# Kernel tuning notes

Hardware: AMD Instinct MI355X
Metric: run time of the kernel (lower is better)

Reference implementation:

```python
import jax, jax.numpy as jnp
import numpy as np
import math

HEADS = 4
DIM_HEAD = 32
EPS = 1e-5

def _ln_channels(x):
    # LayerNorm over channel axis (axis=1) of NCHW, no affine (eps=1e-5)
    mu = jnp.mean(x, axis=1, keepdims=True)
    var = jnp.mean((x - mu) ** 2, axis=1, keepdims=True)
    return (x - mu) * jax.lax.rsqrt(var + EPS)

def setup_inputs() -> dict:
    key = jax.random.key(0)
    k1, k2, k3, k4 = jax.random.split(key, 4)
    dim, inner = 256, HEADS * DIM_HEAD
    x = jax.random.normal(k1, (16, dim, 64, 64), dtype=jnp.float32)
    Wqkv = jax.random.normal(k2, (3 * inner, dim), dtype=jnp.float32) * (1.0 / math.sqrt(dim))
    Wout = jax.random.normal(k3, (dim, inner), dtype=jnp.float32) * (1.0 / math.sqrt(inner))
    bout = jax.random.normal(k4, (dim,), dtype=jnp.float32) * 0.01
    return {"x": x, "Wqkv": Wqkv, "Wout": Wout, "bout": bout}

def reference(x, Wqkv, Wout, bout):
    B, C, H, W = x.shape
    N = H * W
    inner = HEADS * DIM_HEAD
    # pre-norm (channel-wise LayerNorm via permute in torch)
    normed = _ln_channels(x)
    # 1x1 conv to qkv: [B, 3*inner, H, W]
    qkv = jnp.einsum('oc,bchw->bohw', Wqkv, normed)
    q, k, v = jnp.split(qkv, 3, axis=1)
    # [B, inner, H, W] -> [B, heads, N, dim_head]
    def to_heads(t):
        return t.reshape(B, HEADS, DIM_HEAD, N).transpose(0, 1, 3, 2)
    q, k, v = to_heads(q), to_heads(k), to_heads(v)
    q = jax.nn.softmax(q, axis=-1)          # over dim_head
    k = jax.nn.softmax(k, axis=-2)          # over N
    q = q / math.sqrt(DIM_HEAD)
    v = v / N
    context = jnp.einsum('bhnd,bhne->bhde', k, v)   # [B,h,d,d]
    out = jnp.einsum('bhde,bhnd->bhne', context, q) # [B,h,N,d]
    out = out.transpose(0, 1, 3, 2).reshape(B, inner, H, W)
    out = jnp.einsum('oc,bchw->bohw', Wout, out) + bout[None, :, None, None]
    out = _ln_channels(out)                  # LinearAttention.out_norm
    return out + x                           # residual
```

## Files before the change

kernel.cpp:

```cpp
#include <hip/hip_runtime.h>
#include <hip/hip_bf16.h>
#include <math.h>

#define BATCH 16
#define CH 256
#define NPOS 4096
#define INNER 128
#define HEADS 4
#define DH 32

typedef __hip_bfloat16 bf16;
typedef short bf8v __attribute__((ext_vector_type(8)));
typedef float f32x4 __attribute__((ext_vector_type(4)));

__device__ __forceinline__ float b2f(bf16 v) { return __bfloat162float(v); }
__device__ __forceinline__ float us2f(unsigned short u) {
    unsigned w = ((unsigned)u) << 16; float f; __builtin_memcpy(&f, &w, 4); return f;
}
__device__ __forceinline__ unsigned short f2us(float f) {
    bf16 h = __float2bfloat16(f); unsigned short u; __builtin_memcpy(&u, &h, 2); return u;
}
__device__ __forceinline__ bf16 f2b(float v) { return __float2bfloat16(v); }

__global__ __launch_bounds__(256)
void fused_qkv_kernel(const float* __restrict__ x, const float* __restrict__ Wqkv,
                      bf16* __restrict__ p, bf16* __restrict__ kvt) {
    __shared__ bf16 A[128 * 264];
    __shared__ bf16 Bb[128 * 32];
    __shared__ float stats[512];

    const int b = blockIdx.y, n0 = blockIdx.x * 128;
    const int tid = threadIdx.x;
    const int wave = tid >> 6, lane = tid & 63;
    const int wm = (wave >> 1) * 64, wn = (wave & 1) * 64;
    const int lrow = lane & 15, kq = lane >> 4;

    {
        const int n = tid & 127, chalf = tid >> 7;
        const float* xp = x + ((size_t)b * CH + chalf * 128) * NPOS + n0 + n;
        float s = 0.f, sq = 0.f;
        for (int i0 = 0; i0 < 128; i0 += 8) {
            bf8v bv;
            #pragma unroll
            for (int j = 0; j < 8; ++j) {
                float v = xp[(size_t)(i0 + j) * NPOS];
                s += v; sq += v * v;
                bv[j] = (short)f2us(v);
            }
            *(bf8v*)&A[n * 264 + chalf * 128 + i0] = bv;
        }
        stats[tid * 2] = s; stats[tid * 2 + 1] = sq;
    }
    __syncthreads();
    if (tid < 128) {
        float s  = stats[tid * 2] + stats[(tid + 128) * 2];
        float sq = stats[tid * 2 + 1] + stats[(tid + 128) * 2 + 1];
        float m = s * (1.f / 256.f);
        float var = sq * (1.f / 256.f) - m * m;
        stats[tid * 2] = m;
        stats[tid * 2 + 1] = rsqrtf(var + 1e-5f);
    }
    __syncthreads();
    {
        unsigned* A32 = (unsigned*)A;
        #pragma unroll 4
        for (int i = 0; i < 64; ++i) {
            int idx = i * 256 + tid;
            int c2 = idx & 127, n = idx >> 7;
            unsigned u = A32[n * 132 + c2];
            float m = stats[n * 2], rs = stats[n * 2 + 1];
            float v0 = (us2f((unsigned short)(u & 0xffffu)) - m) * rs;
            float v1 = (us2f((unsigned short)(u >> 16)) - m) * rs;
            A32[n * 132 + c2] = (unsigned)f2us(v0) | ((unsigned)f2us(v1) << 16);
        }
    }

    for (int ph = 0; ph < 3; ++ph) {
        const int colbase = (ph == 2) ? 0 : (ph + 1) * 128;
        f32x4 acc[4][4];
        #pragma unroll
        for (int i = 0; i < 4; ++i)
            #pragma unroll
            for (int j = 0; j < 4; ++j) acc[i][j] = (f32x4){0.f, 0.f, 0.f, 0.f};

        for (int k0 = 0; k0 < 256; k0 += 32) {
            __syncthreads();
            #pragma unroll
            for (int i = 0; i < 4; ++i) {
                int s = i * 256 + tid;
                int col = s >> 3, q4 = s & 7;
                float4 w = *(const float4*)&Wqkv[(size_t)(colbase + col) * 256 + k0 + q4 * 4];
                ushort4 wb;
                wb.x = f2us(w.x); wb.y = f2us(w.y); wb.z = f2us(w.z); wb.w = f2us(w.w);
                *(ushort4*)&Bb[col * 32 + q4 * 4] = wb;
            }
            __syncthreads();
            bf8v af[4], bfr[4];
            #pragma unroll
            for (int t = 0; t < 4; ++t)
                af[t] = *(const bf8v*)&A[(wm + t * 16 + lrow) * 264 + k0 + kq * 8];
            #pragma unroll
            for (int t = 0; t < 4; ++t)
                bfr[t] = *(const bf8v*)&Bb[(wn + t * 16 + lrow) * 32 + kq * 8];
            #pragma unroll
            for (int mt = 0; mt < 4; ++mt)
                #pragma unroll
                for (int nt = 0; nt < 4; ++nt)
                    acc[mt][nt] = __builtin_amdgcn_mfma_f32_16x16x32_bf16(
                        af[mt], bfr[nt], acc[mt][nt], 0, 0, 0);
        }

        if (ph < 2) {
            unsigned* B32 = (unsigned*)Bb;
            unsigned* kv32 = (unsigned*)kvt;
            for (int pr = 0; pr < 4; ++pr) {
                __syncthreads();
                if ((wave >> 1) == (pr >> 1)) {
                    int mtb = (pr & 1) * 2;
                    #pragma unroll
                    for (int mi = 0; mi < 2; ++mi) {
                        int mt = mtb + mi;
                        #pragma unroll
                        for (int nt = 0; nt < 4; ++nt)
                            #pragma unroll
                            for (int r = 0; r < 4; ++r) {
                                int rl = mi * 16 + kq * 4 + r;
                                Bb[rl * 128 + wn + nt * 16 + lrow] = f2b(acc[mt][nt][r]);
                            }
                    }
                }
                __syncthreads();
                #pragma unroll
                for (int i = 0; i < 8; ++i) {
                    int idx = i * 256 + tid;
                    int c2 = idx & 63, rl = idx >> 6;
                    kv32[(size_t)(b * NPOS + n0 + pr * 32 + rl) * 128 + ph * 64 + c2] =
                        B32[rl * 64 + c2];
                }
            }
        } else {
            __syncthreads();
            bf16* pt = A;
            #pragma unroll
            for (int mt = 0; mt < 4; ++mt)
                #pragma unroll
                for (int nt = 0; nt < 4; ++nt)
                    #pragma unroll
                    for (int r = 0; r < 4; ++r)
                        pt[(wm + mt * 16 + kq * 4 + r) * 132 + wn + nt * 16 + lrow] =
                            f2b(acc[mt][nt][r]);
            __syncthreads();
            {
                int row = tid >> 1, hp = (tid & 1) * 2;
                float s0 = 0.f, s1 = 0.f;
                #pragma unroll 8
                for (int j = 0; j < 32; ++j) s0 += __expf(b2f(pt[row * 132 + hp * 32 + j]));
                #pragma unroll 8
                for (int j = 0; j < 32; ++j) s1 += __expf(b2f(pt[row * 132 + hp * 32 + 32 + j]));
                stats[row * 4 + hp] = 1.f / s0;
                stats[row * 4 + hp + 1] = 1.f / s1;
            }
            __syncthreads();
            unsigned* pt32 = (unsigned*)pt;
            unsigned* pg32 = (unsigned*)p;
            #pragma unroll 4
            for (int i = 0; i < 32; ++i) {
                int idx = i * 256 + tid;
                int c2 = idx & 63, n = idx >> 6;
                unsigned u = pt32[n * 66 + c2];
                float rd = stats[n * 4 + (c2 >> 4)];
                float v0 = __expf(us2f((unsigned short)(u & 0xffffu))) * rd;
                float v1 = __expf(us2f((unsigned short)(u >> 16))) * rd;
                pg32[(size_t)(b * NPOS + n0 + n) * 64 + c2] =
                    (unsigned)f2us(v0) | ((unsigned)f2us(v1) << 16);
            }
        }
    }
}

__global__ __launch_bounds__(256)
void context_kernel(const bf16* __restrict__ kvt, float* __restrict__ ctxu,
                    float* __restrict__ separt) {
    __shared__ float ks[128][36];
    __shared__ float vs[128][36];
    __shared__ float red_se[4][32];
    int sp = blockIdx.x, h = blockIdx.y, b = blockIdx.z;
    int tid = threadIdx.x;
    int wave = tid >> 6, lane = tid & 63;
    int eg = lane & 7, dg = lane >> 3;
    int sd = tid & 31, sq = (tid >> 5) & 3;
    const int koff = h * DH, voff = 128 + h * DH;
    size_t rowbase = ((size_t)b * NPOS + sp * 1024) * 256;

    float acc[4][4] = {};
    float se_loc = 0.f;

    for (int nc = 0; nc < 1024; nc += 128) {
        for (int t = tid; t < 1024; t += 256) {
            int n = t >> 3, dq = t & 7;
            const bf16* row = kvt + rowbase + (size_t)(nc + n) * 256;
            ushort4 ku = *(const ushort4*)(row + koff + dq * 4);
            ushort4 vu = *(const ushort4*)(row + voff + dq * 4);
            f32x4 kf, vf;
            kf[0] = __expf(us2f(ku.x)); kf[1] = __expf(us2f(ku.y));
            kf[2] = __expf(us2f(ku.z)); kf[3] = __expf(us2f(ku.w));
            vf[0] = us2f(vu.x); vf[1] = us2f(vu.y); vf[2] = us2f(vu.z); vf[3] = us2f(vu.w);
            *(f32x4*)&ks[n][dq * 4] = kf;
            *(f32x4*)&vs[n][dq * 4] = vf;
        }
        __syncthreads();
        #pragma unroll 4
        for (int i = 0; i < 32; ++i) {
            int n = wave * 32 + i;
            f32x4 kv = *(const f32x4*)&ks[n][dg * 4];
            f32x4 vv = *(const f32x4*)&vs[n][eg * 4];
            #pragma unroll
            for (int j = 0; j < 4; ++j)
                #pragma unroll
                for (int i2 = 0; i2 < 4; ++i2)
                    acc[j][i2] += kv[j] * vv[i2];
        }
        if (tid < 128) {
            float s = 0.f;
            #pragma unroll 8
            for (int i = 0; i < 32; ++i) s += ks[sq * 32 + i][sd];
            se_loc += s;
        }
        __syncthreads();
    }

    if (tid < 128) red_se[sq][sd] = se_loc;
    float* red = &ks[0][0];
    #pragma unroll
    for (int j = 0; j < 4; ++j)
        #pragma unroll
        for (int i = 0; i < 4; ++i)
            red[(wave * 64 + lane) * 16 + j * 4 + i] = acc[j][i];
    __syncthreads();
    size_t bhsp = ((size_t)(b * HEADS + h) * 4 + sp);
    for (int idx = tid; idx < 1024; idx += 256) {
        int d = idx >> 5, e = idx & 31;
        int l = (d >> 2) * 8 + (e >> 2);
        int slot = (d & 3) * 4 + (e & 3);
        float s = 0.f;
        #pragma unroll
        for (int w = 0; w < 4; ++w) s += red[(w * 64 + l) * 16 + slot];
        ctxu[bhsp * 1024 + idx] = s;
    }
    if (tid < 32) {
        float s = red_se[0][tid] + red_se[1][tid] + red_se[2][tid] + red_se[3][tid];
        separt[bhsp * 32 + tid] = s;
    }
}

__global__ __launch_bounds__(256)
void wmod_kernel(const float* __restrict__ Wout, const float* __restrict__ ctxu,
                 const float* __restrict__ separt, bf16* __restrict__ wmod) {
    __shared__ float cs[4096];
    __shared__ float ses[128];
    int cg = blockIdx.x, b = blockIdx.y;
    int tid = threadIdx.x;
    for (int idx = tid; idx < 4096; idx += 256) {
        int hh = idx >> 10, rest = idx & 1023;
        float s = 0.f;
        #pragma unroll
        for (int sp = 0; sp < 4; ++sp)
            s += ctxu[(((size_t)(b * HEADS + hh) * 4) + sp) * 1024 + rest];
        cs[idx] = s;
    }
    if (tid < 128) {
        int hh = tid >> 5, d = tid & 31;
        float s = 0.f;
        #pragma unroll
        for (int sp = 0; sp < 4; ++sp)
            s += separt[(((size_t)(b * HEADS + hh) * 4) + sp) * 32 + d];
        ses[tid] = s;
    }
    __syncthreads();
    int c = cg * 32 + (tid & 31);
    int g = tid >> 5;
    int h = g >> 1, d0 = (g & 1) * 16;
    const float* wr = Wout + (size_t)c * INNER + h * DH;
    float w[32];
    #pragma unroll
    for (int i = 0; i < 8; ++i) {
        float4 t = *(const float4*)&wr[i * 4];
        w[i * 4] = t.x; w[i * 4 + 1] = t.y; w[i * 4 + 2] = t.z; w[i * 4 + 3] = t.w;
    }
    const float SCALE = 4.3158341e-05f;
    #pragma unroll
    for (int dd = 0; dd < 16; ++dd) {
        int d = d0 + dd;
        const float* cr = &cs[h * 1024 + d * 32];
        float s = 0.f;
        #pragma unroll
        for (int e4 = 0; e4 < 8; ++e4) {
            f32x4 t = *(const f32x4*)&cr[e4 * 4];
            s += w[e4 * 4] * t[0] + w[e4 * 4 + 1] * t[1]
               + w[e4 * 4 + 2] * t[2] + w[e4 * 4 + 3] * t[3];
        }
        float val = s * SCALE / ses[h * 32 + d];
        wmod[((size_t)b * CH + c) * INNER + h * DH + d] = f2b(val);
    }
}

__global__ __launch_bounds__(256)
void fused_out_kernel(const bf16* __restrict__ p, const bf16* __restrict__ wmod,
                      const float* __restrict__ bout, const float* __restrict__ x,
                      float* __restrict__ out) {
    __shared__ char lds[51200];
    bf16* Ap = (bf16*)lds;
    bf16* Bw = (bf16*)(lds + 34816);
    float* ct = (float*)lds;
    float* st = (float*)(lds + 34816);

    const int b = blockIdx.y, n0 = blockIdx.x * 128;
    const int tid = threadIdx.x;
    const int wave = tid >> 6, lane = tid & 63;
    const int wm = (wave >> 1) * 64, wn2 = (wave & 1) * 128;
    const int lrow = lane & 15, kq = lane >> 4;

    {
        const unsigned* pg32 = (const unsigned*)p;
        unsigned* A32 = (unsigned*)Ap;
        #pragma unroll 4
        for (int i = 0; i < 32; ++i) {
            int idx = i * 256 + tid;
            int c2 = idx & 63, n = idx >> 6;
            A32[n * 68 + c2] = pg32[(size_t)(b * NPOS + n0 + n) * 64 + c2];
        }
    }

    f32x4 acc[4][8];
    #pragma unroll
    for (int i = 0; i < 4; ++i)
        #pragma unroll
        for (int j = 0; j < 8; ++j) acc[i][j] = (f32x4){0.f, 0.f, 0.f, 0.f};

    const bf16* wb = wmod + (size_t)b * CH * INNER;
    for (int k0 = 0; k0 < 128; k0 += 32) {
        __syncthreads();
        #pragma unroll
        for (int i = 0; i < 4; ++i) {
            int s = i * 256 + tid;
            int col = s >> 2, q4 = s & 3;
            uint4 u = *(const uint4*)&wb[(size_t)col * 128 + k0 + q4 * 8];
            *(uint4*)&Bw[col * 32 + q4 * 8] = u;
        }
        __syncthreads();
        bf8v af[4], bfr[8];
        #pragma unroll
        for (int t = 0; t < 4; ++t)
            af[t] = *(const bf8v*)&Ap[(wm + t * 16 + lrow) * 136 + k0 + kq * 8];
        #pragma unroll
        for (int t = 0; t < 8; ++t)
            bfr[t] = *(const bf8v*)&Bw[(wn2 + t * 16 + lrow) * 32 + kq * 8];
        #pragma unroll
        for (int mt = 0; mt < 4; ++mt)
            #pragma unroll
            for (int nt = 0; nt < 8; ++nt)
                acc[mt][nt] = __builtin_amdgcn_mfma_f32_16x16x32_bf16(
                    af[mt], bfr[nt], acc[mt][nt], 0, 0, 0);
    }

    #pragma unroll
    for (int nt = 0; nt < 8; ++nt) {
        float bv = bout[wn2 + nt * 16 + lrow];
        #pragma unroll
        for (int mt = 0; mt < 4; ++mt)
            #pragma unroll
            for (int r = 0; r < 4; ++r) acc[mt][nt][r] += bv;
    }

    __syncthreads();
    #pragma unroll
    for (int mt = 0; mt < 4; ++mt)
        #pragma unroll
        for (int r = 0; r < 4; ++r) {
            float s = 0.f, sq = 0.f;
            #pragma unroll
            for (int nt = 0; nt < 8; ++nt) {
                float v = acc[mt][nt][r];
                s += v; sq += v * v;
            }
            #pragma unroll
            for (int m = 1; m <= 8; m <<= 1) {
                s += __shfl_xor(s, m, 64);
                sq += __shfl_xor(sq, m, 64);
            }
            if (lrow == 0) {
                int row = wm + mt * 16 + kq * 4 + r;
                st[(wave & 1) * 256 + row * 2] = s;
                st[(wave & 1) * 256 + row * 2 + 1] = sq;
            }
        }
    __syncthreads();
    if (tid < 128) {
        float s  = st[tid * 2] + st[256 + tid * 2];
        float sq = st[tid * 2 + 1] + st[256 + tid * 2 + 1];
        float m = s * (1.f / 256.f);
        float var = sq * (1.f / 256.f) - m * m;
        st[512 + tid * 2] = m;
        st[512 + tid * 2 + 1] = rsqrtf(var + 1e-5f);
    }
    __syncthreads();
    #pragma unroll
    for (int mt = 0; mt < 4; ++mt)
        #pragma unroll
        for (int r = 0; r < 4; ++r) {
            int row = wm + mt * 16 + kq * 4 + r;
            float m = st[512 + row * 2], rs = st[512 + row * 2 + 1];
            #pragma unroll
            for (int nt = 0; nt < 8; ++nt)
                acc[mt][nt][r] = (acc[mt][nt][r] - m) * rs;
        }

    for (int pr = 0; pr < 4; ++pr) {
        __syncthreads();
        if ((wave >> 1) == (pr >> 1)) {
            int mtb = (pr & 1) * 2;
            #pragma unroll
            for (int mi = 0; mi < 2; ++mi) {
                int mt = mtb + mi;
                #pragma unroll
                for (int nt = 0; nt < 8; ++nt)
                    #pragma unroll
                    for (int r = 0; r < 4; ++r) {
                        int rl = mi * 16 + kq * 4 + r;
                        ct[(wn2 + nt * 16 + lrow) * 33 + rl] = acc[mt][nt][r];
                    }
            }
        }
        __syncthreads();
        #pragma unroll 4
        for (int i = 0; i < 32; ++i) {
            int idx = i * 256 + tid;
            int n = idx & 31, c = idx >> 5;
            size_t gi = ((size_t)b * CH + c) * NPOS + n0 + pr * 32 + n;
            out[gi] = ct[c * 33 + n] + x[gi];
        }
    }
}

extern "C" void kernel_launch(void* const* d_in, const int* in_sizes, int n_in,
                              void* d_out, int out_size, void* d_ws, size_t ws_size,
                              hipStream_t stream) {
    const float* x    = (const float*)d_in[0];
    const float* Wqkv = (const float*)d_in[1];
    const float* Wout = (const float*)d_in[2];
    const float* bout = (const float*)d_in[3];
    float* out = (float*)d_out;

    char* ws = (char*)d_ws;
    bf16*  p      = (bf16*)ws;
    bf16*  kvt    = (bf16*)(ws + 16777216);
    float* ctxu   = (float*)(ws + 50331648);
    float* separt = (float*)(ws + 51380224);
    bf16*  wmod   = (bf16*)(ws + 51412992);

    fused_qkv_kernel<<<dim3(32, BATCH), 256, 0, stream>>>(x, Wqkv, p, kvt);
    context_kernel<<<dim3(4, HEADS, BATCH), 256, 0, stream>>>(kvt, ctxu, separt);
    wmod_kernel<<<dim3(8, BATCH), 256, 0, stream>>>(Wout, ctxu, separt, wmod);
    fused_out_kernel<<<dim3(32, BATCH), 256, 0, stream>>>(p, wmod, bout, x, out);
}
```

Baseline: 225.6 us.

## Pre-convert Wqkv to bf16 and read GEMM B fragments directly from global

Adds a small kernel that converts Wqkv to bf16 once into a workspace buffer that aliases ctxu, which is safe because ctxu is written only later by context_kernel. Both GEMM kernels now load their weight fragments straight from global/L2 into registers, skipping the LDS staging and the two barriers per k-step. This removes per-block fp32-to-bf16 conversion and the synchronisation stalls, and shrinks LDS in the output kernel, which may raise occupancy. The cost is uncoalesced 16-byte global loads for each fragment, plus one extra kernel launch.

```diff
diff --git a/kernel.cpp b/kernel.cpp
--- a/kernel.cpp
+++ b/kernel.cpp
@@ -23,7 +23,16 @@
 __device__ __forceinline__ bf16 f2b(float v) { return __float2bfloat16(v); }
 
 __global__ __launch_bounds__(256)
-void fused_qkv_kernel(const float* __restrict__ x, const float* __restrict__ Wqkv,
+void prep_w_kernel(const float* __restrict__ Wqkv, bf16* __restrict__ wqb) {
+    int idx = (blockIdx.x * 256 + threadIdx.x) * 4;
+    float4 w = *(const float4*)&Wqkv[idx];
+    ushort4 u;
+    u.x = f2us(w.x); u.y = f2us(w.y); u.z = f2us(w.z); u.w = f2us(w.w);
+    *(ushort4*)&wqb[idx] = u;
+}
+
+__global__ __launch_bounds__(256)
+void fused_qkv_kernel(const float* __restrict__ x, const bf16* __restrict__ wqb,
                       bf16* __restrict__ p, bf16* __restrict__ kvt) {
     __shared__ bf16 A[128 * 264];
     __shared__ bf16 Bb[128 * 32];
@@ -74,34 +83,26 @@
             A32[n * 132 + c2] = (unsigned)f2us(v0) | ((unsigned)f2us(v1) << 16);
         }
     }
+    __syncthreads();
 
     for (int ph = 0; ph < 3; ++ph) {
         const int colbase = (ph == 2) ? 0 : (ph + 1) * 128;
+        const bf16* wp = wqb + (size_t)colbase * 256;
         f32x4 acc[4][4];
         #pragma unroll
         for (int i = 0; i < 4; ++i)
             #pragma unroll
             for (int j = 0; j < 4; ++j) acc[i][j] = (f32x4){0.f, 0.f, 0.f, 0.f};
 
+        #pragma unroll 2
         for (int k0 = 0; k0 < 256; k0 += 32) {
-            __syncthreads();
-            #pragma unroll
-            for (int i = 0; i < 4; ++i) {
-                int s = i * 256 + tid;
-                int col = s >> 3, q4 = s & 7;
-                float4 w = *(const float4*)&Wqkv[(size_t)(colbase + col) * 256 + k0 + q4 * 4];
-                ushort4 wb;
-                wb.x = f2us(w.x); wb.y = f2us(w.y); wb.z = f2us(w.z); wb.w = f2us(w.w);
-                *(ushort4*)&Bb[col * 32 + q4 * 4] = wb;
-            }
-            __syncthreads();
             bf8v af[4], bfr[4];
             #pragma unroll
             for (int t = 0; t < 4; ++t)
                 af[t] = *(const bf8v*)&A[(wm + t * 16 + lrow) * 264 + k0 + kq * 8];
             #pragma unroll
             for (int t = 0; t < 4; ++t)
-                bfr[t] = *(const bf8v*)&Bb[(wn + t * 16 + lrow) * 32 + kq * 8];
+                bfr[t] = *(const bf8v*)&wp[(size_t)(wn + t * 16 + lrow) * 256 + k0 + kq * 8];
             #pragma unroll
             for (int mt = 0; mt < 4; ++mt)
                 #pragma unroll
@@ -308,9 +309,8 @@
 void fused_out_kernel(const bf16* __restrict__ p, const bf16* __restrict__ wmod,
                       const float* __restrict__ bout, const float* __restrict__ x,
                       float* __restrict__ out) {
-    __shared__ char lds[51200];
+    __shared__ char lds[37888];
     bf16* Ap = (bf16*)lds;
-    bf16* Bw = (bf16*)(lds + 34816);
     float* ct = (float*)lds;
     float* st = (float*)(lds + 34816);
 
@@ -330,6 +330,7 @@
             A32[n * 68 + c2] = pg32[(size_t)(b * NPOS + n0 + n) * 64 + c2];
         }
     }
+    __syncthreads();
 
     f32x4 acc[4][8];
     #pragma unroll
@@ -338,23 +339,15 @@
         for (int j = 0; j < 8; ++j) acc[i][j] = (f32x4){0.f, 0.f, 0.f, 0.f};
 
     const bf16* wb = wmod + (size_t)b * CH * INNER;
+    #pragma unroll 2
     for (int k0 = 0; k0 < 128; k0 += 32) {
-        __syncthreads();
-        #pragma unroll
-        for (int i = 0; i < 4; ++i) {
-            int s = i * 256 + tid;
-            int col = s >> 2, q4 = s & 3;
-            uint4 u = *(const uint4*)&wb[(size_t)col * 128 + k0 + q4 * 8];
-            *(uint4*)&Bw[col * 32 + q4 * 8] = u;
-        }
-        __syncthreads();
         bf8v af[4], bfr[8];
         #pragma unroll
         for (int t = 0; t < 4; ++t)
             af[t] = *(const bf8v*)&Ap[(wm + t * 16 + lrow) * 136 + k0 + kq * 8];
         #pragma unroll
         for (int t = 0; t < 8; ++t)
-            bfr[t] = *(const bf8v*)&Bw[(wn2 + t * 16 + lrow) * 32 + kq * 8];
+            bfr[t] = *(const bf8v*)&wb[(size_t)(wn2 + t * 16 + lrow) * 128 + k0 + kq * 8];
         #pragma unroll
         for (int mt = 0; mt < 4; ++mt)
             #pragma unroll
@@ -372,7 +365,6 @@
             for (int r = 0; r < 4; ++r) acc[mt][nt][r] += bv;
     }
 
-    __syncthreads();
     #pragma unroll
     for (int mt = 0; mt < 4; ++mt)
         #pragma unroll
@@ -457,8 +449,10 @@
     float* ctxu   = (float*)(ws + 50331648);
     float* separt = (float*)(ws + 51380224);
     bf16*  wmod   = (bf16*)(ws + 51412992);
-
-    fused_qkv_kernel<<<dim3(32, BATCH), 256, 0, stream>>>(x, Wqkv, p, kvt);
+    bf16*  wqb    = (bf16*)(ws + 50331648);
+
+    prep_w_kernel<<<dim3(96), 256, 0, stream>>>(Wqkv, wqb);
+    fused_qkv_kernel<<<dim3(32, BATCH), 256, 0, stream>>>(x, wqb, p, kvt);
     context_kernel<<<dim3(4, HEADS, BATCH), 256, 0, stream>>>(kvt, ctxu, separt);
     wmod_kernel<<<dim3(8, BATCH), 256, 0, stream>>>(Wout, ctxu, separt, wmod);
     fused_out_kernel<<<dim3(32, BATCH), 256, 0, stream>>>(p, wmod, bout, x, out);
```

Result: slower. 233.7 us (+3.6%).
